# Kernel tuning notes

Measured on AMD Instinct MI355X. Metric: run time of the kernel, lower is better.

## Reference

```python
import jax, jax.numpy as jnp
import numpy as np
from jax import lax

S, B, K, T = 16, 16, 3, 20
FP, DP = 64, 28
CP = FP - DP + 1            # 37
P = CP * CP                 # 1369 == num_pixels
H, Hh, D = 256, 128, 2


def setup_inputs() -> dict:
    key = jax.random.key(0)
    ks = jax.random.split(key, 20)

    def lin_w(k, fan_in, fan_out):
        return jax.random.normal(k, (fan_in, fan_out), jnp.float32) / np.sqrt(fan_in)

    inp = {
        "frames": jax.random.uniform(ks[0], (B, T, FP, FP), jnp.float32),
        "digit": jax.random.uniform(ks[1], (S, B, K, DP, DP), jnp.float32),
        # enc_hidden: Linear(P, H)
        "w_h1": lin_w(ks[2], P, H), "b_h1": jnp.zeros((H,), jnp.float32),
        # where_mean: Linear(H, Hh) -> ReLU -> Linear(Hh, D) -> Tanh
        "wm1": lin_w(ks[3], H, Hh), "bm1": jnp.zeros((Hh,), jnp.float32),
        "wm2": lin_w(ks[4], Hh, D), "bm2": jnp.zeros((D,), jnp.float32),
        # where_log_std: Linear(H, Hh) -> ReLU -> Linear(Hh, D)
        "ws1": lin_w(ks[5], H, Hh), "bs1": jnp.zeros((Hh,), jnp.float32),
        "ws2": lin_w(ks[6], Hh, D), "bs2": jnp.zeros((D,), jnp.float32),
        # disp_mean: Linear(P, H) -> ReLU -> Linear(H, Hh) -> ReLU -> Linear(Hh, D) -> Tanh
        "wd1": lin_w(ks[7], P, H), "bd1": jnp.zeros((H,), jnp.float32),
        "wd2": lin_w(ks[8], H, Hh), "bd2": jnp.zeros((Hh,), jnp.float32),
        "wd3": lin_w(ks[9], Hh, D), "bd3": jnp.zeros((D,), jnp.float32),
    }
    return inp


def _lin(x, w, b):
    return x @ w + b


def _forward(frames, digit, w_h1, b_h1, wm1, bm1, wm2, bm2,
             ws1, bs1, ws2, bs2, wd1, bd1, wd2, bd2, wd3, bd3):
    # frames: (B, T, FP, FP); digit: (S, B, K, DP, DP)
    s, b, k_ = digit.shape[0], digit.shape[1], digit.shape[2]
    t = frames.shape[1]

    # Template correlation. The original builds a (T, S*B*K, FP, FP) repeated
    # input and runs conv2d with groups=S*B*K. Since frames do not depend on
    # (s, k), the identical math is a grouped conv with groups=B where group b
    # holds the S*K templates for batch element b.
    x = frames.transpose(1, 0, 2, 3)                          # (T, B, FP, FP)
    kern = digit.transpose(1, 0, 2, 3, 4).reshape(b * s * k_, 1, DP, DP)
    conv = lax.conv_general_dilated(
        x, kern, window_strides=(1, 1), padding='VALID',
        dimension_numbers=('NCHW', 'OIHW', 'NCHW'),
        feature_group_count=b)                                # (T, B*S*K, CP, CP)
    cp = conv.shape[-1]
    conv = conv.reshape(t, b, s, k_, cp * cp)
    conv = conv.transpose(2, 1, 0, 3, 4)                      # (S, B, T, K, P)

    # temporal displacement of correlation maps
    conv_disp = conv[:, :, 1:] - conv[:, :, :-1]              # (S, B, T-1, K, P)

    # disp_mean MLP
    d = jax.nn.relu(_lin(conv_disp, wd1, bd1))
    d = jax.nn.relu(_lin(d, wd2, bd2))
    disp = jnp.tanh(_lin(d, wd3, bd3))                        # (S, B, T-1, K, D)

    # enc_hidden on softmax-normalized correlation maps
    hidden = jax.nn.relu(_lin(jax.nn.softmax(conv, axis=-1), w_h1, b_h1))

    q_mean = jnp.tanh(_lin(jax.nn.relu(_lin(hidden, wm1, bm1)), wm2, bm2))
    q_std = jnp.exp(_lin(jax.nn.relu(_lin(hidden, ws1, bs1)), ws2, bs2))
    return q_mean, q_std, disp


def reference(frames, digit, w_h1, b_h1, wm1, bm1, wm2, bm2,
              ws1, bs1, ws2, bs2, wd1, bd1, wd2, bd2, wd3, bd3):
    return _forward(frames, digit, w_h1, b_h1, wm1, bm1, wm2, bm2,
                    ws1, bs1, ws2, bs2, wd1, bd1, wd2, bd2, wd3, bd3)
```

## Files before the change

### kernel.cpp

```cpp
#include <hip/hip_runtime.h>
#include <hip/hip_fp16.h>

typedef __attribute__((ext_vector_type(8))) _Float16 half8;
typedef __attribute__((ext_vector_type(2))) _Float16 h2f;
typedef __attribute__((ext_vector_type(4))) float f32x4;

#define NP 1369
#define KP 1376
#define NKT 43
#define ROWS_A 15360
#define ROWS_D 14592

#define PA_OFF   0
#define PD_OFF   (ROWS_A * KP)
#define PWH_OFF  (PD_OFF + ROWS_D * KP)
#define PWD_OFF  (PWH_OFF + NKT * 16 * 512)
#define PW2_OFF  (PWD_OFF + NKT * 16 * 512)
#define PWD2_OFF (PW2_OFF + 8 * 16 * 512)
#define TSUM_OFF (PWD2_OFF + 8 * 8 * 512)
#define STAT_OFF (TSUM_OFF + 1536)

__device__ __forceinline__ unsigned short f2h(float f) {
    __half h = __float2half(f);
    return __half_as_ushort(h);
}
__device__ __forceinline__ h2f u2h2(unsigned int u) {
    h2f r; __builtin_memcpy(&r, &u, 4); return r;
}

__global__ __launch_bounds__(256)
void k0_pack(const float* __restrict__ w_h1, const float* __restrict__ wd1,
             const float* __restrict__ wm1,  const float* __restrict__ ws1,
             const float* __restrict__ wd2,  const float* __restrict__ digit,
             unsigned short* __restrict__ wsu, float* __restrict__ tsum)
{
    const int tid = threadIdx.x;
    if (blockIdx.x >= 3136) {
        const int sbk = (blockIdx.x - 3136) * 4 + (tid >> 6);
        const int l = tid & 63;
        const float* tp = digit + (size_t)sbk * 784;
        float s = 0.f;
        for (int i = l; i < 784; i += 64) s += tp[i];
        for (int o = 32; o; o >>= 1) s += __shfl_xor(s, o, 64);
        if (l == 0) tsum[sbk] = 0.5f * s;
        return;
    }
    int idx = blockIdx.x * 256 + tid;
    int local, mode;
    unsigned short* dst;
    if (idx < 352256)      { mode = 0; local = idx;          dst = wsu + PWH_OFF; }
    else if (idx < 704512) { mode = 1; local = idx - 352256; dst = wsu + PWD_OFF; }
    else if (idx < 770048) { mode = 2; local = idx - 704512; dst = wsu + PW2_OFF; }
    else                   { mode = 3; local = idx - 770048; dst = wsu + PWD2_OFF; }
    int j = local & 7, lane = (local >> 3) & 63, rest = local >> 9;
    int NTn = (mode == 3) ? 8 : 16;
    int nt = rest % NTn, kt = rest / NTn;
    int k = kt * 32 + ((lane >> 4) << 3) + j;
    int n = nt * 16 + (lane & 15);
    float v = 0.f;
    if (mode == 0)      { if (k < NP) v = w_h1[k * 256 + n]; }
    else if (mode == 1) { if (k < NP) v = wd1[k * 256 + n]; }
    else if (mode == 2) { v = (n < 128) ? wm1[k * 128 + n] : ws1[k * 128 + (n - 128)]; }
    else                { v = wd2[k * 128 + n]; }
    dst[local] = f2h(v);
}

__global__ __launch_bounds__(512)
void k1a_corr(const float* __restrict__ frames, const float* __restrict__ digit,
              const float* __restrict__ tsum, unsigned short* __restrict__ wsu)
{
    __shared__ __align__(16) unsigned short Bs[14 * 3 * 512];
    __shared__ __align__(16) unsigned int frd[64 * 36];
    __shared__ float Cn[48];

    const int tid = threadIdx.x, l = tid & 63, w = tid >> 6;
    const int mh = blockIdx.x & 1;
    const int bt = blockIdx.x >> 1;
    const int t  = bt % 20;
    const int bb = bt / 20;

    if (tid < 48) {
        int sbk_n = ((tid / 3) * 16 + bb) * 3 + (tid % 3);
        Cn[tid] = tsum[sbk_n];
    }
    if (tid < 256) frd[(tid >> 2) * 36 + 32 + (tid & 3)] = 0u;
    {
        const float4* fp4 = (const float4*)(frames + (size_t)(bb * 20 + t) * 4096);
        for (int idx = tid; idx < 1024; idx += 512) {
            float4 v = fp4[idx];
            int r = idx >> 4, c4 = idx & 15;
            unsigned lo = (unsigned)f2h(v.x) | ((unsigned)f2h(v.y) << 16);
            unsigned hi = (unsigned)f2h(v.z) | ((unsigned)f2h(v.w) << 16);
            *(uint2*)&frd[r * 36 + c4 * 2] = make_uint2(lo, hi);
        }
    }

    const int c15 = l & 15, quad = l >> 4, v0q = quad << 3;
    const int cnt = (50 - w) / 8;

    int baseb[6]; unsigned shv[6];
#pragma unroll
    for (int it = 0; it < 6; ++it) {
        int tI = mh * 43 + w + 8 * it;
        int p  = tI * 16 + c15;
        int pc = p > 1368 ? 1368 : p;
        int i  = pc / 37;
        int jj = pc - i * 37;
        int c  = jj + v0q;
        baseb[it] = i * 144 + (c >> 1) * 4;
        shv[it]   = (unsigned)((c & 1) << 4);
    }
    f32x4 acc[6][3];
#pragma unroll
    for (int it = 0; it < 6; ++it)
#pragma unroll
        for (int nt = 0; nt < 3; ++nt) acc[it][nt] = (f32x4){0.f, 0.f, 0.f, 0.f};

    for (int ph = 0; ph < 2; ++ph) {
        __syncthreads();
        for (int s = tid; s < 2688; s += 512) {
            int ktl = s / 192;
            int rem = s - ktl * 192;
            int nt = rem >> 6, sl = rem & 63;
            int nl = nt * 16 + (sl & 15);
            int v0 = (sl >> 4) << 3;
            int kt = ph * 14 + ktl;
            int sbk_n = ((nl / 3) * 16 + bb) * 3 + (nl % 3);
            const float* tp = digit + (size_t)sbk_n * 784 + kt * 28 + v0;
            float4 fa = *(const float4*)tp;
            float4 fb = (v0 <= 16) ? *(const float4*)(tp + 4) : make_float4(0.f, 0.f, 0.f, 0.f);
            uint4 pk;
            pk.x = (unsigned)f2h(fa.x) | ((unsigned)f2h(fa.y) << 16);
            pk.y = (unsigned)f2h(fa.z) | ((unsigned)f2h(fa.w) << 16);
            pk.z = (unsigned)f2h(fb.x) | ((unsigned)f2h(fb.y) << 16);
            pk.w = (unsigned)f2h(fb.z) | ((unsigned)f2h(fb.w) << 16);
            *(uint4*)(Bs + s * 8) = pk;
        }
        __syncthreads();

        for (int ktl = 0; ktl < 14; ++ktl) {
            const int kt = ph * 14 + ktl;
            half8 bf0 = *(const half8*)(Bs + ktl * 1536 + 0 * 512 + l * 8);
            half8 bf1 = *(const half8*)(Bs + ktl * 1536 + 1 * 512 + l * 8);
            half8 bf2 = *(const half8*)(Bs + ktl * 1536 + 2 * 512 + l * 8);
            const char* fbase = (const char*)frd + kt * 144;
#pragma unroll
            for (int it = 0; it < 6; ++it) {
                if (it < cnt) {
                    const char* ap = fbase + baseb[it];
                    unsigned w0 = *(const unsigned*)(ap);
                    unsigned w1 = *(const unsigned*)(ap + 4);
                    unsigned w2 = *(const unsigned*)(ap + 8);
                    unsigned w3 = *(const unsigned*)(ap + 12);
                    unsigned w4 = *(const unsigned*)(ap + 16);
                    unsigned sh = shv[it];
                    union { unsigned u[4]; half8 h8; } af;
                    af.u[0] = (unsigned)(((((unsigned long long)w1) << 32) | w0) >> sh);
                    af.u[1] = (unsigned)(((((unsigned long long)w2) << 32) | w1) >> sh);
                    af.u[2] = (unsigned)(((((unsigned long long)w3) << 32) | w2) >> sh);
                    af.u[3] = (unsigned)(((((unsigned long long)w4) << 32) | w3) >> sh);
                    acc[it][0] = __builtin_amdgcn_mfma_f32_16x16x32_f16(af.h8, bf0, acc[it][0], 0, 0, 0);
                    acc[it][1] = __builtin_amdgcn_mfma_f32_16x16x32_f16(af.h8, bf1, acc[it][1], 0, 0, 0);
                    acc[it][2] = __builtin_amdgcn_mfma_f32_16x16x32_f16(af.h8, bf2, acc[it][2], 0, 0, 0);
                }
            }
        }
    }
#pragma unroll
    for (int it = 0; it < 6; ++it) {
        if (it < cnt) {
            int tI = mh * 43 + w + 8 * it;
            int p0 = tI * 16 + quad * 4;
#pragma unroll
            for (int nt = 0; nt < 3; ++nt) {
                int nl = nt * 16 + c15;
                int sbk_n = ((nl / 3) * 16 + bb) * 3 + (nl % 3);
                const float C = Cn[nl];
                unsigned short* orow = wsu + PA_OFF + (size_t)(sbk_n * 20 + t) * KP;
                if (p0 + 3 <= 1368) {
                    ushort4 st;
                    st.x = f2h(acc[it][nt][0] - C); st.y = f2h(acc[it][nt][1] - C);
                    st.z = f2h(acc[it][nt][2] - C); st.w = f2h(acc[it][nt][3] - C);
                    *(ushort4*)(orow + p0) = st;
                } else {
#pragma unroll
                    for (int r = 0; r < 4; ++r)
                        if (p0 + r <= 1368) orow[p0 + r] = f2h(acc[it][nt][r] - C);
                }
            }
        }
    }
}

__global__ __launch_bounds__(256)
void k1b_stats(const unsigned short* __restrict__ wsu, float2* __restrict__ stats)
{
    const int l = threadIdx.x & 63, wv = threadIdx.x >> 6;
    const int row = blockIdx.x * 4 + wv;
    const unsigned* rp = (const unsigned*)(wsu + PA_OFF + (size_t)row * KP);

    float f0[11], f1[11];
    float mx = -3.0e38f;
#pragma unroll
    for (int i = 0; i < 11; ++i) {
        int q = l + i * 64;
        unsigned u = (q < 685) ? rp[q] : 0u;
        h2f h = u2h2(u);
        f0[i] = (q < 685) ? (float)h[0] : -3.0e38f;
        f1[i] = (q < 684) ? (float)h[1] : -3.0e38f;
        mx = fmaxf(mx, fmaxf(f0[i], f1[i]));
    }
    for (int o = 32; o; o >>= 1) mx = fmaxf(mx, __shfl_xor(mx, o, 64));
    float sum = 0.f;
#pragma unroll
    for (int i = 0; i < 11; ++i)
        sum += __expf(f0[i] - mx) + __expf(f1[i] - mx);
    for (int o = 32; o; o >>= 1) sum += __shfl_xor(sum, o, 64);
    if (l == 0) stats[row] = make_float2(mx, 1.0f / sum);
}

__global__ __launch_bounds__(256)
void k2_gemmAB(unsigned short* __restrict__ wsu, const float* __restrict__ b_h1,
               const float2* __restrict__ stats)
{
    __shared__ __align__(16) unsigned short Bbuf[2][2 * 8192];

    const int tid = threadIdx.x, l = tid & 63, w = tid >> 6;
    const int c15 = l & 15, quad = l >> 4;
    const int M0 = blockIdx.x * 64;
    unsigned short* Abase = wsu + PA_OFF;
    const unsigned short* PWH = wsu + PWH_OFF;
    const unsigned short* PWD = wsu + PWD_OFF;
    float* HR = (float*)(wsu + PD_OFF);

    const bool isH = (w < 2);
    const int rt0 = M0 + (w & 1) * 32;
    const int row0 = rt0 + c15, row1 = rt0 + 16 + c15;
    const unsigned short* a0p = Abase + (size_t)row0 * KP + quad * 8;
    const unsigned short* a1p = Abase + (size_t)row1 * KP + quad * 8;
    float2 st0 = make_float2(0.f, 0.f), st1 = make_float2(0.f, 0.f);
    if (isH) { st0 = stats[row0]; st1 = stats[row1]; }

    f32x4 acc[2][16];
#pragma unroll
    for (int m = 0; m < 2; ++m)
#pragma unroll
        for (int n = 0; n < 16; ++n) acc[m][n] = (f32x4){0.f, 0.f, 0.f, 0.f};

    {
        const int4* sH = (const int4*)(PWH);
        const int4* sD = (const int4*)(PWD);
        int4* dH = (int4*)(Bbuf[0]);
        int4* dD = (int4*)(Bbuf[0] + 8192);
#pragma unroll
        for (int c = 0; c < 4; ++c) {
            dH[tid + 256 * c] = sH[tid + 256 * c];
            dD[tid + 256 * c] = sD[tid + 256 * c];
        }
    }
    half8 curA0 = *(const half8*)(a0p);
    half8 curA1 = *(const half8*)(a1p);
    __syncthreads();

    for (int kt = 0; kt < NKT; ++kt) {
        const int db = kt & 1;
        half8 nxtA0 = curA0, nxtA1 = curA1;
        if (kt + 1 < NKT) {
            nxtA0 = *(const half8*)(a0p + (kt + 1) * 32);
            nxtA1 = *(const half8*)(a1p + (kt + 1) * 32);
        }
        int4 rH[4], rD[4];
        if (kt + 1 < NKT) {
            const int4* sH = (const int4*)(PWH + (size_t)(kt + 1) * 8192);
            const int4* sD = (const int4*)(PWD + (size_t)(kt + 1) * 8192);
#pragma unroll
            for (int c = 0; c < 4; ++c) {
                rH[c] = sH[tid + 256 * c];
                rD[c] = sD[tid + 256 * c];
            }
        }
        half8 afA = curA0, afB = curA1;
        if (isH) {
            union { half8 h8; unsigned u[4]; } ia, ib, oa, ob;
            ia.h8 = afA; ib.h8 = afB;
#pragma unroll
            for (int q = 0; q < 4; ++q) {
                h2f ha = u2h2(ia.u[q]);
                h2f hb = u2h2(ib.u[q]);
                float a0 = __expf((float)ha[0] - st0.x) * st0.y;
                float a1 = __expf((float)ha[1] - st0.x) * st0.y;
                float b0 = __expf((float)hb[0] - st1.x) * st1.y;
                float b1 = __expf((float)hb[1] - st1.x) * st1.y;
                oa.u[q] = (unsigned)f2h(a0) | ((unsigned)f2h(a1) << 16);
                ob.u[q] = (unsigned)f2h(b0) | ((unsigned)f2h(b1) << 16);
            }
            afA = oa.h8; afB = ob.h8;
        }
        const unsigned short* bb = Bbuf[db] + (isH ? 0 : 8192);
#pragma unroll
        for (int nt = 0; nt < 16; ++nt) {
            half8 bf = *(const half8*)(bb + nt * 512 + l * 8);
            acc[0][nt] = __builtin_amdgcn_mfma_f32_16x16x32_f16(afA, bf, acc[0][nt], 0, 0, 0);
            acc[1][nt] = __builtin_amdgcn_mfma_f32_16x16x32_f16(afB, bf, acc[1][nt], 0, 0, 0);
        }
        if (kt + 1 < NKT) {
            int4* dH = (int4*)(Bbuf[db ^ 1]);
            int4* dD = (int4*)(Bbuf[db ^ 1] + 8192);
#pragma unroll
            for (int c = 0; c < 4; ++c) {
                dH[tid + 256 * c] = rH[c];
                dD[tid + 256 * c] = rD[c];
            }
        }
        curA0 = nxtA0; curA1 = nxtA1;
        __syncthreads();
    }

    if (isH) {
#pragma unroll
        for (int nt = 0; nt < 16; ++nt) {
            const int col = nt * 16 + c15;
            const float bv = b_h1[col];
#pragma unroll
            for (int m = 0; m < 2; ++m)
#pragma unroll
                for (int r = 0; r < 4; ++r) {
                    const int row = rt0 + m * 16 + quad * 4 + r;
                    float v = acc[m][nt][r] + bv;
                    Abase[(size_t)row * KP + col] = f2h(v > 0.f ? v : 0.f);
                }
        }
    } else {
#pragma unroll
        for (int nt = 0; nt < 16; ++nt) {
            const int col = nt * 16 + c15;
#pragma unroll
            for (int m = 0; m < 2; ++m)
#pragma unroll
                for (int r = 0; r < 4; ++r) {
                    const int row = rt0 + m * 16 + quad * 4 + r;
                    HR[(size_t)row * 256 + col] = acc[m][nt][r];
                }
        }
    }
}

template <bool PATHA>
__global__ __launch_bounds__(256)
void k2_heads(unsigned short* __restrict__ wsu,
              const float* __restrict__ b1a, const float* __restrict__ b1b,
              const float* __restrict__ w2a, const float* __restrict__ b2a,
              const float* __restrict__ w2b, const float* __restrict__ b2b,
              const float* __restrict__ bd1, float* __restrict__ out)
{
    constexpr int NT2 = PATHA ? 16 : 8;
    constexpr int NI4 = NT2 / 4;
    __shared__ __align__(16) unsigned short Bsh[2][NT2 * 512];
    const int tid = threadIdx.x, l = tid & 63, w = tid >> 6;
    const int c = l & 15, quad = l >> 4;
    const int M0 = blockIdx.x * 64;
    const unsigned short* PW = wsu + (PATHA ? PW2_OFF : PWD2_OFF);

    f32x4 acc[NT2];
#pragma unroll
    for (int n = 0; n < NT2; ++n) acc[n] = (f32x4){0.f, 0.f, 0.f, 0.f};

    const int row = M0 + w * 16 + c;
    const unsigned short* arow = nullptr;
    const float* h1p = nullptr; const float* h0p = nullptr;
    if (PATHA) {
        arow = wsu + PA_OFF + (size_t)row * KP + quad * 8;
    } else {
        const float* HR = (const float*)(wsu + PD_OFF);
        const int sbk = row / 19, dt = row % 19;
        h0p = HR + (size_t)(sbk * 20 + dt) * 256 + quad * 8;
        h1p = h0p + 256;
    }

    {
        const int4* src = (const int4*)(PW);
        int4* dst = (int4*)Bsh[0];
#pragma unroll
        for (int cc = 0; cc < NI4; ++cc)
            dst[tid + 256 * cc] = src[tid + 256 * cc];
    }
    half8 curPA = {};
    float4 c1a = {}, c1b = {}, c0a = {}, c0b = {};
    if (PATHA) {
        curPA = *(const half8*)(arow);
    } else {
        c1a = *(const float4*)(h1p); c1b = *(const float4*)(h1p + 4);
        c0a = *(const float4*)(h0p); c0b = *(const float4*)(h0p + 4);
    }
    __syncthreads();

    for (int kt = 0; kt < 8; ++kt) {
        const int db = kt & 1;
        half8 nxtPA = curPA;
        float4 n1a = c1a, n1b = c1b, n0a = c0a, n0b = c0b;
        if (kt + 1 < 8) {
            if (PATHA) {
                nxtPA = *(const half8*)(arow + (kt + 1) * 32);
            } else {
                n1a = *(const float4*)(h1p + (kt + 1) * 32);
                n1b = *(const float4*)(h1p + (kt + 1) * 32 + 4);
                n0a = *(const float4*)(h0p + (kt + 1) * 32);
                n0b = *(const float4*)(h0p + (kt + 1) * 32 + 4);
            }
        }
        int4 rB[NI4];
        if (kt + 1 < 8) {
            const int4* src = (const int4*)(PW + (size_t)(kt + 1) * (NT2 * 512));
#pragma unroll
            for (int cc = 0; cc < NI4; ++cc) rB[cc] = src[tid + 256 * cc];
        }
        half8 af;
        if (PATHA) {
            af = curPA;
        } else {
            float4 bb = *(const float4*)(bd1 + kt * 32 + quad * 8);
            float4 bb2 = *(const float4*)(bd1 + kt * 32 + quad * 8 + 4);
            float v0 = fmaxf(c1a.x - c0a.x + bb.x, 0.f);
            float v1 = fmaxf(c1a.y - c0a.y + bb.y, 0.f);
            float v2 = fmaxf(c1a.z - c0a.z + bb.z, 0.f);
            float v3 = fmaxf(c1a.w - c0a.w + bb.w, 0.f);
            float v4 = fmaxf(c1b.x - c0b.x + bb2.x, 0.f);
            float v5 = fmaxf(c1b.y - c0b.y + bb2.y, 0.f);
            float v6 = fmaxf(c1b.z - c0b.z + bb2.z, 0.f);
            float v7 = fmaxf(c1b.w - c0b.w + bb2.w, 0.f);
            union { unsigned u[4]; half8 h8; } pk;
            pk.u[0] = (unsigned)f2h(v0) | ((unsigned)f2h(v1) << 16);
            pk.u[1] = (unsigned)f2h(v2) | ((unsigned)f2h(v3) << 16);
            pk.u[2] = (unsigned)f2h(v4) | ((unsigned)f2h(v5) << 16);
            pk.u[3] = (unsigned)f2h(v6) | ((unsigned)f2h(v7) << 16);
            af = pk.h8;
        }
#pragma unroll
        for (int nt = 0; nt < NT2; ++nt) {
            half8 bf = *(const half8*)(Bsh[db] + nt * 512 + l * 8);
            acc[nt] = __builtin_amdgcn_mfma_f32_16x16x32_f16(af, bf, acc[nt], 0, 0, 0);
        }
        if (kt + 1 < 8) {
            int4* dst = (int4*)Bsh[db ^ 1];
#pragma unroll
            for (int cc = 0; cc < NI4; ++cc) dst[tid + 256 * cc] = rB[cc];
        }
        curPA = nxtPA;
        c1a = n1a; c1b = n1b; c0a = n0a; c0b = n0b;
        __syncthreads();
    }
#pragma unroll
    for (int nt = 0; nt < NT2; ++nt) {
        float bv;
        if (PATHA) bv = (nt < 8) ? b1a[nt * 16 + c] : b1b[(nt - 8) * 16 + c];
        else       bv = b1a[nt * 16 + c];
#pragma unroll
        for (int r = 0; r < 4; ++r) {
            float v = acc[nt][r] + bv;
            acc[nt][r] = v > 0.f ? v : 0.f;
        }
    }
    float pm[2][4], ps[2][4];
#pragma unroll
    for (int d = 0; d < 2; ++d)
#pragma unroll
        for (int r = 0; r < 4; ++r) { pm[d][r] = 0.f; ps[d][r] = 0.f; }
#pragma unroll
    for (int d = 0; d < 2; ++d)
#pragma unroll
        for (int nt = 0; nt < 8; ++nt) {
            const float wmv = w2a[(nt * 16 + c) * 2 + d];
            float wsv = 0.f;
            if (PATHA) wsv = w2b[(nt * 16 + c) * 2 + d];
#pragma unroll
            for (int r = 0; r < 4; ++r) {
                pm[d][r] = fmaf(acc[nt][r], wmv, pm[d][r]);
                if (PATHA) ps[d][r] = fmaf(acc[nt + 8][r], wsv, ps[d][r]);
            }
        }
#pragma unroll
    for (int o = 1; o < 16; o <<= 1)
#pragma unroll
        for (int d = 0; d < 2; ++d)
#pragma unroll
            for (int r = 0; r < 4; ++r) {
                pm[d][r] += __shfl_xor(pm[d][r], o, 64);
                if (PATHA) ps[d][r] += __shfl_xor(ps[d][r], o, 64);
            }
    if (c == 0) {
#pragma unroll
        for (int r = 0; r < 4; ++r) {
            const int orow = M0 + w * 16 + quad * 4 + r;
            if (PATHA) {
                const int sbk = orow / 20, t = orow % 20;
                const int sb = sbk / 3, kk = sbk % 3;
                const int oi = ((sb * 20 + t) * 3 + kk) * 2;
                out[oi + 0] = tanhf(pm[0][r] + b2a[0]);
                out[oi + 1] = tanhf(pm[1][r] + b2a[1]);
                out[30720 + oi + 0] = __expf(ps[0][r] + b2b[0]);
                out[30720 + oi + 1] = __expf(ps[1][r] + b2b[1]);
            } else {
                const int sbk = orow / 19, dt = orow % 19;
                const int sb = sbk / 3, kk = sbk % 3;
                const int oi = 61440 + ((sb * 19 + dt) * 3 + kk) * 2;
                out[oi + 0] = tanhf(pm[0][r] + b2a[0]);
                out[oi + 1] = tanhf(pm[1][r] + b2a[1]);
            }
        }
    }
}

extern "C" void kernel_launch(void* const* d_in, const int* in_sizes, int n_in,
                              void* d_out, int out_size, void* d_ws, size_t ws_size,
                              hipStream_t stream) {
    const float* frames = (const float*)d_in[0];
    const float* digit  = (const float*)d_in[1];
    const float* w_h1   = (const float*)d_in[2];
    const float* b_h1   = (const float*)d_in[3];
    const float* wm1    = (const float*)d_in[4];
    const float* bm1    = (const float*)d_in[5];
    const float* wm2    = (const float*)d_in[6];
    const float* bm2    = (const float*)d_in[7];
    const float* ws1    = (const float*)d_in[8];
    const float* bs1    = (const float*)d_in[9];
    const float* ws2    = (const float*)d_in[10];
    const float* bs2    = (const float*)d_in[11];
    const float* wd1    = (const float*)d_in[12];
    const float* bd1    = (const float*)d_in[13];
    const float* wd2    = (const float*)d_in[14];
    const float* bd2    = (const float*)d_in[15];
    const float* wd3    = (const float*)d_in[16];
    const float* bd3    = (const float*)d_in[17];

    unsigned short* wsu = (unsigned short*)d_ws;
    float* tsum = (float*)(wsu + TSUM_OFF);
    float2* stats = (float2*)(wsu + STAT_OFF);
    float* o = (float*)d_out;

    k0_pack<<<dim3(3328), dim3(256), 0, stream>>>(w_h1, wd1, wm1, ws1, wd2, digit, wsu, tsum);
    k1a_corr<<<dim3(640), dim3(512), 0, stream>>>(frames, digit, tsum, wsu);
    k1b_stats<<<dim3(3840), dim3(256), 0, stream>>>(wsu, stats);
    k2_gemmAB<<<dim3(240), dim3(256), 0, stream>>>(wsu, b_h1, stats);
    k2_heads<true><<<dim3(240), dim3(256), 0, stream>>>(wsu, bm1, bs1, wm2, bm2, ws2, bs2, nullptr, o);
    k2_heads<false><<<dim3(228), dim3(256), 0, stream>>>(wsu, bd2, nullptr, wd3, bd3, nullptr, nullptr, bd1, o);
}
```

Baseline: 149.4 us.

## Stage corr output through LDS for coalesced stores; double waves in gemmAB

```diff
diff --git a/kernel.cpp b/kernel.cpp
--- a/kernel.cpp
+++ b/kernel.cpp
@@ -166,28 +166,30 @@
             }
         }
     }
-#pragma unroll
-    for (int it = 0; it < 6; ++it) {
-        if (it < cnt) {
-            int tI = mh * 43 + w + 8 * it;
-            int p0 = tI * 16 + quad * 4;
+
+    for (int itg = 0; itg < 6; ++itg) {
+        __syncthreads();
+        if (itg < cnt) {
 #pragma unroll
             for (int nt = 0; nt < 3; ++nt) {
-                int nl = nt * 16 + c15;
-                int sbk_n = ((nl / 3) * 16 + bb) * 3 + (nl % 3);
+                const int nl = nt * 16 + c15;
                 const float C = Cn[nl];
-                unsigned short* orow = wsu + PA_OFF + (size_t)(sbk_n * 20 + t) * KP;
-                if (p0 + 3 <= 1368) {
-                    ushort4 st;
-                    st.x = f2h(acc[it][nt][0] - C); st.y = f2h(acc[it][nt][1] - C);
-                    st.z = f2h(acc[it][nt][2] - C); st.w = f2h(acc[it][nt][3] - C);
-                    *(ushort4*)(orow + p0) = st;
-                } else {
-#pragma unroll
-                    for (int r = 0; r < 4; ++r)
-                        if (p0 + r <= 1368) orow[p0 + r] = f2h(acc[it][nt][r] - C);
-                }
-            }
+                ushort4 st;
+                st.x = f2h(acc[itg][nt][0] - C);
+                st.y = f2h(acc[itg][nt][1] - C);
+                st.z = f2h(acc[itg][nt][2] - C);
+                st.w = f2h(acc[itg][nt][3] - C);
+                *(ushort4*)(Bs + nl * 136 + w * 16 + quad * 4) = st;
+            }
+        }
+        __syncthreads();
+        const int nseg = (itg == 5) ? 6 : 16;
+        for (int i = tid; i < 48 * nseg; i += 512) {
+            int rowl = i / nseg, seg = i - rowl * nseg;
+            int sbk_n = ((rowl / 3) * 16 + bb) * 3 + (rowl % 3);
+            uint4 v = *(const uint4*)(Bs + rowl * 136 + seg * 8);
+            *(uint4*)(wsu + PA_OFF + (size_t)(sbk_n * 20 + t) * KP
+                      + mh * 688 + itg * 128 + seg * 8) = v;
         }
     }
 }
@@ -219,7 +221,7 @@
     if (l == 0) stats[row] = make_float2(mx, 1.0f / sum);
 }
 
-__global__ __launch_bounds__(256)
+__global__ __launch_bounds__(512)
 void k2_gemmAB(unsigned short* __restrict__ wsu, const float* __restrict__ b_h1,
                const float2* __restrict__ stats)
 {
@@ -233,19 +235,16 @@
     const unsigned short* PWD = wsu + PWD_OFF;
     float* HR = (float*)(wsu + PD_OFF);
 
-    const bool isH = (w < 2);
-    const int rt0 = M0 + (w & 1) * 32;
-    const int row0 = rt0 + c15, row1 = rt0 + 16 + c15;
+    const bool isH = (w < 4);
+    const int wl = w & 3;
+    const int row0 = M0 + wl * 16 + c15;
     const unsigned short* a0p = Abase + (size_t)row0 * KP + quad * 8;
-    const unsigned short* a1p = Abase + (size_t)row1 * KP + quad * 8;
-    float2 st0 = make_float2(0.f, 0.f), st1 = make_float2(0.f, 0.f);
-    if (isH) { st0 = stats[row0]; st1 = stats[row1]; }
-
-    f32x4 acc[2][16];
-#pragma unroll
-    for (int m = 0; m < 2; ++m)
-#pragma unroll
-        for (int n = 0; n < 16; ++n) acc[m][n] = (f32x4){0.f, 0.f, 0.f, 0.f};
+    float2 st0 = make_float2(0.f, 0.f);
+    if (isH) st0 = stats[row0];
+
+    f32x4 acc[16];
+#pragma unroll
+    for (int n = 0; n < 16; ++n) acc[n] = (f32x4){0.f, 0.f, 0.f, 0.f};
 
     {
         const int4* sH = (const int4*)(PWH);
@@ -253,66 +252,57 @@
         int4* dH = (int4*)(Bbuf[0]);
         int4* dD = (int4*)(Bbuf[0] + 8192);
 #pragma unroll
-        for (int c = 0; c < 4; ++c) {
-            dH[tid + 256 * c] = sH[tid + 256 * c];
-            dD[tid + 256 * c] = sD[tid + 256 * c];
-        }
-    }
-    half8 curA0 = *(const half8*)(a0p);
-    half8 curA1 = *(const half8*)(a1p);
+        for (int c = 0; c < 2; ++c) {
+            dH[tid + 512 * c] = sH[tid + 512 * c];
+            dD[tid + 512 * c] = sD[tid + 512 * c];
+        }
+    }
+    half8 curA = *(const half8*)(a0p);
     __syncthreads();
 
     for (int kt = 0; kt < NKT; ++kt) {
         const int db = kt & 1;
-        half8 nxtA0 = curA0, nxtA1 = curA1;
-        if (kt + 1 < NKT) {
-            nxtA0 = *(const half8*)(a0p + (kt + 1) * 32);
-            nxtA1 = *(const half8*)(a1p + (kt + 1) * 32);
-        }
-        int4 rH[4], rD[4];
+        half8 nxtA = curA;
+        if (kt + 1 < NKT) nxtA = *(const half8*)(a0p + (kt + 1) * 32);
+        int4 rH[2], rD[2];
         if (kt + 1 < NKT) {
             const int4* sH = (const int4*)(PWH + (size_t)(kt + 1) * 8192);
             const int4* sD = (const int4*)(PWD + (size_t)(kt + 1) * 8192);
 #pragma unroll
-            for (int c = 0; c < 4; ++c) {
-                rH[c] = sH[tid + 256 * c];
-                rD[c] = sD[tid + 256 * c];
-            }
-        }
-        half8 afA = curA0, afB = curA1;
+            for (int c = 0; c < 2; ++c) {
+                rH[c] = sH[tid + 512 * c];
+                rD[c] = sD[tid + 512 * c];
+            }
+        }
+        half8 af = curA;
         if (isH) {
-            union { half8 h8; unsigned u[4]; } ia, ib, oa, ob;
-            ia.h8 = afA; ib.h8 = afB;
+            union { half8 h8; unsigned u[4]; } ia, oa;
+            ia.h8 = af;
 #pragma unroll
             for (int q = 0; q < 4; ++q) {
                 h2f ha = u2h2(ia.u[q]);
-                h2f hb = u2h2(ib.u[q]);
                 float a0 = __expf((float)ha[0] - st0.x) * st0.y;
                 float a1 = __expf((float)ha[1] - st0.x) * st0.y;
-                float b0 = __expf((float)hb[0] - st1.x) * st1.y;
-                float b1 = __expf((float)hb[1] - st1.x) * st1.y;
                 oa.u[q] = (unsigned)f2h(a0) | ((unsigned)f2h(a1) << 16);
-                ob.u[q] = (unsigned)f2h(b0) | ((unsigned)f2h(b1) << 16);
-            }
-            afA = oa.h8; afB = ob.h8;
+            }
+            af = oa.h8;
         }
         const unsigned short* bb = Bbuf[db] + (isH ? 0 : 8192);
 #pragma unroll
         for (int nt = 0; nt < 16; ++nt) {
             half8 bf = *(const half8*)(bb + nt * 512 + l * 8);
-            acc[0][nt] = __builtin_amdgcn_mfma_f32_16x16x32_f16(afA, bf, acc[0][nt], 0, 0, 0);
-            acc[1][nt] = __builtin_amdgcn_mfma_f32_16x16x32_f16(afB, bf, acc[1][nt], 0, 0, 0);
+            acc[nt] = __builtin_amdgcn_mfma_f32_16x16x32_f16(af, bf, acc[nt], 0, 0, 0);
         }
         if (kt + 1 < NKT) {
             int4* dH = (int4*)(Bbuf[db ^ 1]);
             int4* dD = (int4*)(Bbuf[db ^ 1] + 8192);
 #pragma unroll
-            for (int c = 0; c < 4; ++c) {
-                dH[tid + 256 * c] = rH[c];
-                dD[tid + 256 * c] = rD[c];
-            }
-        }
-        curA0 = nxtA0; curA1 = nxtA1;
+            for (int c = 0; c < 2; ++c) {
+                dH[tid + 512 * c] = rH[c];
+                dD[tid + 512 * c] = rD[c];
+            }
+        }
+        curA = nxtA;
         __syncthreads();
     }
 
@@ -322,25 +312,21 @@
             const int col = nt * 16 + c15;
             const float bv = b_h1[col];
 #pragma unroll
-            for (int m = 0; m < 2; ++m)
-#pragma unroll
-                for (int r = 0; r < 4; ++r) {
-                    const int row = rt0 + m * 16 + quad * 4 + r;
-                    float v = acc[m][nt][r] + bv;
-                    Abase[(size_t)row * KP + col] = f2h(v > 0.f ? v : 0.f);
-                }
+            for (int r = 0; r < 4; ++r) {
+                const int row = M0 + wl * 16 + quad * 4 + r;
+                float v = acc[nt][r] + bv;
+                Abase[(size_t)row * KP + col] = f2h(v > 0.f ? v : 0.f);
+            }
         }
     } else {
 #pragma unroll
         for (int nt = 0; nt < 16; ++nt) {
             const int col = nt * 16 + c15;
 #pragma unroll
-            for (int m = 0; m < 2; ++m)
-#pragma unroll
-                for (int r = 0; r < 4; ++r) {
-                    const int row = rt0 + m * 16 + quad * 4 + r;
-                    HR[(size_t)row * 256 + col] = acc[m][nt][r];
-                }
+            for (int r = 0; r < 4; ++r) {
+                const int row = M0 + wl * 16 + quad * 4 + r;
+                HR[(size_t)row * 256 + col] = acc[nt][r];
+            }
         }
     }
 }
@@ -540,7 +526,7 @@
     k0_pack<<<dim3(3328), dim3(256), 0, stream>>>(w_h1, wd1, wm1, ws1, wd2, digit, wsu, tsum);
     k1a_corr<<<dim3(640), dim3(512), 0, stream>>>(frames, digit, tsum, wsu);
     k1b_stats<<<dim3(3840), dim3(256), 0, stream>>>(wsu, stats);
-    k2_gemmAB<<<dim3(240), dim3(256), 0, stream>>>(wsu, b_h1, stats);
+    k2_gemmAB<<<dim3(240), dim3(512), 0, stream>>>(wsu, b_h1, stats);
     k2_heads<true><<<dim3(240), dim3(256), 0, stream>>>(wsu, bm1, bs1, wm2, bm2, ws2, bs2, nullptr, o);
     k2_heads<false><<<dim3(228), dim3(256), 0, stream>>>(wsu, bd2, nullptr, wd3, bd3, nullptr, nullptr, bd1, o);
 }
```

Result: faster. 138.7 us (-7.1%).
